# Performance work log

Measured on AMD Instinct MI355X. Metric: run time of the kernel, lower is better.

The kernel has to match this reference:

```python
import jax, jax.numpy as jnp
import numpy as np

B, N, E = 64, 128, 262144
HID, NRBF, NBLK = 128, 64, 4
RCUT = 6.0
GAMMA = 10.0 / (RCUT * RCUT)


def setup_inputs() -> dict:
    key = jax.random.key(0)
    ks = jax.random.split(key, 20)
    s_rbf = 1.0 / np.sqrt(NRBF)
    s_hid = 1.0 / np.sqrt(HID)
    return {
        "Z": jax.random.randint(ks[0], (B, N), 0, 100),
        "pos": jax.random.normal(ks[1], (B, N, 3), dtype=jnp.float32) * 3.0,
        "edge_index": jax.random.randint(ks[2], (2, E), 0, B * N),
        "embed_w": jax.random.normal(ks[3], (100, HID), dtype=jnp.float32) * 0.02,
        "edge_w1": jax.random.normal(ks[4], (NBLK, NRBF, HID), dtype=jnp.float32) * s_rbf,
        "edge_b1": jnp.zeros((NBLK, HID), dtype=jnp.float32),
        "edge_w2": jax.random.normal(ks[5], (NBLK, HID, HID), dtype=jnp.float32) * s_hid,
        "edge_b2": jnp.zeros((NBLK, HID), dtype=jnp.float32),
        "lin_in_w": jax.random.normal(ks[6], (NBLK, HID, HID), dtype=jnp.float32) * s_hid,
        "node_w1": jax.random.normal(ks[7], (NBLK, HID, HID), dtype=jnp.float32) * s_hid,
        "node_b1": jnp.zeros((NBLK, HID), dtype=jnp.float32),
        "node_w2": jax.random.normal(ks[8], (NBLK, HID, HID), dtype=jnp.float32) * s_hid,
        "node_b2": jnp.zeros((NBLK, HID), dtype=jnp.float32),
        "ln_g": jnp.ones((NBLK, HID), dtype=jnp.float32),
        "ln_b": jnp.zeros((NBLK, HID), dtype=jnp.float32),
        "ro_w1": jax.random.normal(ks[9], (HID, HID // 2), dtype=jnp.float32) * s_hid,
        "ro_b1": jnp.zeros((HID // 2,), dtype=jnp.float32),
        "ro_w2": jax.random.normal(ks[10], (HID // 2, 1), dtype=jnp.float32) * (1.0 / np.sqrt(HID // 2)),
        "ro_b2": jnp.zeros((1,), dtype=jnp.float32),
    }


def _layernorm(x, g, b, eps=1e-5):
    mu = x.mean(-1, keepdims=True)
    var = ((x - mu) ** 2).mean(-1, keepdims=True)
    return (x - mu) / jnp.sqrt(var + eps) * g + b


def reference(Z, pos, edge_index, embed_w, edge_w1, edge_b1, edge_w2, edge_b2,
              lin_in_w, node_w1, node_b1, node_w2, node_b2, ln_g, ln_b,
              ro_w1, ro_b1, ro_w2, ro_b2):
    Zf = Z.reshape(-1)               # [B*N]
    pf = pos.reshape(-1, 3)          # [B*N, 3]
    src, dst = edge_index[0], edge_index[1]

    h = embed_w[Zf]                  # [B*N, H]

    # edge RBF features
    d = jnp.linalg.norm(pf[src] - pf[dst], axis=-1)      # [E]
    d = jnp.minimum(d, RCUT)
    centers = jnp.linspace(0.0, RCUT, NRBF)
    rbf = jnp.exp(-GAMMA * (d[:, None] - centers) ** 2)  # [E, NRBF]

    for i in range(NBLK):
        # CFConv: edge filter MLP on rbf
        w = jax.nn.silu(rbf @ edge_w1[i] + edge_b1[i]) @ edge_w2[i] + edge_b2[i]  # [E,H]
        m = w * (h[src] @ lin_in_w[i])                                            # [E,H]
        agg = jnp.zeros_like(h).at[dst].add(m)                                    # scatter-add [B*N,H]
        out = jax.nn.silu(agg @ node_w1[i] + node_b1[i]) @ node_w2[i] + node_b2[i]
        h = _layernorm(h + out, ln_g[i], ln_b[i])

    # readout: SiLU -> Linear -> SiLU -> Linear
    x = jax.nn.silu(h) @ ro_w1 + ro_b1
    e_atom = (jax.nn.silu(x) @ ro_w2 + ro_b2)[:, 0]      # [B*N]
    return e_atom.reshape(B, N).sum(axis=-1)             # per-graph energies [B]
```

## Files before the change

kernel.cpp:

```cpp
#include <hip/hip_runtime.h>

#define BN 8192
#define EE 262144
#define HIDD 128
#define NRBF 64
#define NBLK 4
#define TLUT 2048
#define CAP 128
#define MR 16
#define FR 8
#define RCUTF 6.0f
#define GAMMAF (10.0f / 36.0f)

typedef unsigned short u16;
typedef __attribute__((ext_vector_type(8))) short short8x;
typedef __attribute__((ext_vector_type(4))) float f32x4;

__device__ __forceinline__ float silu_f(float v) {
    return v / (1.0f + __expf(-v));
}
__device__ __forceinline__ float bf2f(u16 u) {
    return __uint_as_float(((unsigned)u) << 16);
}
__device__ __forceinline__ u16 f2bf(float f) {
    unsigned u = __float_as_uint(f);
    unsigned r = u + 0x7FFFu + ((u >> 16) & 1u);
    return (u16)(r >> 16);
}

__global__ void k_prep(const float* __restrict__ liw, const float* __restrict__ nw1,
                       const float* __restrict__ nw2, const float* __restrict__ ro1,
                       u16* __restrict__ liwT, u16* __restrict__ nw1T,
                       u16* __restrict__ nw2T, u16* __restrict__ ro1T,
                       int* __restrict__ cnt, float* __restrict__ out, int out_n) {
    int id0 = blockIdx.x * 256 + threadIdx.x;
    for (int id = id0; id < 12 * 16384; id += 65536) {
        int which = id >> 14;
        int r = id & 16383;
        int n = r >> 7, k = r & 127;
        const float* src = which < 4 ? liw : (which < 8 ? nw1 : nw2);
        u16* dst = which < 4 ? liwT : (which < 8 ? nw1T : nw2T);
        int b = which & 3;
        dst[b * 16384 + n * 128 + k] = f2bf(src[(size_t)b * 16384 + k * 128 + n]);
    }
    if (id0 < 8192) {
        cnt[id0] = 0;
        int n = id0 >> 7, k = id0 & 127;
        ro1T[n * 128 + k] = f2bf(ro1[k * 64 + n]);
        if (id0 < out_n) out[id0] = 0.0f;
    }
}

__global__ void k_edges(const int* __restrict__ ei, const float* __restrict__ pos,
                        int* __restrict__ cnt, int* __restrict__ meta) {
    int e = blockIdx.x * 256 + threadIdx.x;
    int s = ei[e];
    int d = ei[EE + e];
    float dx = pos[s * 3 + 0] - pos[d * 3 + 0];
    float dy = pos[s * 3 + 1] - pos[d * 3 + 1];
    float dz = pos[s * 3 + 2] - pos[d * 3 + 2];
    float dist = fminf(sqrtf(dx * dx + dy * dy + dz * dz), RCUTF);
    int i0 = (int)(dist * ((TLUT - 1) / RCUTF) + 0.5f);
    i0 = i0 > TLUT - 1 ? TLUT - 1 : i0;
    int p = atomicAdd(&cnt[d], 1);
    if (p < CAP) meta[(size_t)d * CAP + p] = (i0 << 13) | s;
}

__global__ __launch_bounds__(256) void k_lutall(const float* __restrict__ W1a,
                                                const float* __restrict__ b1a,
                                                const float* __restrict__ W2a,
                                                const float* __restrict__ b2a,
                                                u16* __restrict__ lutall) {
    __shared__ float As[32 * 33];
    __shared__ float Ws[32 * 128];
    __shared__ float T2[32 * 128];
    int net = blockIdx.x >> 6;
    int r0l = (blockIdx.x & 63) * 32;
    const float* W1 = W1a + (size_t)net * NRBF * HIDD;
    const float* b1 = b1a + net * HIDD;
    const float* W2 = W2a + (size_t)net * HIDD * HIDD;
    const float* b2 = b2a + net * HIDD;
    u16* lutp = lutall + (size_t)net * TLUT * HIDD;
    int tid = threadIdx.x;
    int tx = tid & 31, ty = tid >> 5;
    int c0 = tx * 4, rr = ty * 4;
    float acc[4][4] = {};
    for (int kc = 0; kc < NRBF; kc += 32) {
        int lr = tid >> 3, lc = (tid & 7) * 4;
        float dt = (r0l + lr) * (RCUTF / (TLUT - 1));
#pragma unroll
        for (int j = 0; j < 4; ++j) {
            float c = (kc + lc + j) * (RCUTF / 63.0f);
            float u = dt - c;
            As[lr * 33 + lc + j] = __expf(-GAMMAF * u * u);
        }
#pragma unroll
        for (int j = 0; j < 4; ++j) {
            int idx = tid + j * 256;
            int wr = idx >> 5, wc = (idx & 31) * 4;
            *(float4*)&Ws[wr * 128 + wc] =
                *(const float4*)&W1[(size_t)(kc + wr) * HIDD + wc];
        }
        __syncthreads();
#pragma unroll 8
        for (int k = 0; k < 32; ++k) {
            float4 wv = *(float4*)&Ws[k * 128 + c0];
            float a0 = As[(rr + 0) * 33 + k];
            float a1 = As[(rr + 1) * 33 + k];
            float a2 = As[(rr + 2) * 33 + k];
            float a3 = As[(rr + 3) * 33 + k];
            acc[0][0] += a0 * wv.x; acc[0][1] += a0 * wv.y; acc[0][2] += a0 * wv.z; acc[0][3] += a0 * wv.w;
            acc[1][0] += a1 * wv.x; acc[1][1] += a1 * wv.y; acc[1][2] += a1 * wv.z; acc[1][3] += a1 * wv.w;
            acc[2][0] += a2 * wv.x; acc[2][1] += a2 * wv.y; acc[2][2] += a2 * wv.z; acc[2][3] += a2 * wv.w;
            acc[3][0] += a3 * wv.x; acc[3][1] += a3 * wv.y; acc[3][2] += a3 * wv.z; acc[3][3] += a3 * wv.w;
        }
        __syncthreads();
    }
#pragma unroll
    for (int i = 0; i < 4; ++i)
#pragma unroll
        for (int j = 0; j < 4; ++j)
            T2[(rr + i) * 128 + c0 + j] = silu_f(acc[i][j] + b1[c0 + j]);
    float acc2[4][4] = {};
    __syncthreads();
    for (int kc = 0; kc < HIDD; kc += 32) {
#pragma unroll
        for (int j = 0; j < 4; ++j) {
            int idx = tid + j * 256;
            int wr = idx >> 5, wc = (idx & 31) * 4;
            *(float4*)&Ws[wr * 128 + wc] =
                *(const float4*)&W2[(size_t)(kc + wr) * HIDD + wc];
        }
        __syncthreads();
#pragma unroll 8
        for (int k = 0; k < 32; ++k) {
            float4 wv = *(float4*)&Ws[k * 128 + c0];
            float a0 = T2[(rr + 0) * 128 + kc + k];
            float a1 = T2[(rr + 1) * 128 + kc + k];
            float a2 = T2[(rr + 2) * 128 + kc + k];
            float a3 = T2[(rr + 3) * 128 + kc + k];
            acc2[0][0] += a0 * wv.x; acc2[0][1] += a0 * wv.y; acc2[0][2] += a0 * wv.z; acc2[0][3] += a0 * wv.w;
            acc2[1][0] += a1 * wv.x; acc2[1][1] += a1 * wv.y; acc2[1][2] += a1 * wv.z; acc2[1][3] += a1 * wv.w;
            acc2[2][0] += a2 * wv.x; acc2[2][1] += a2 * wv.y; acc2[2][2] += a2 * wv.z; acc2[2][3] += a2 * wv.w;
            acc2[3][0] += a3 * wv.x; acc2[3][1] += a3 * wv.y; acc2[3][2] += a3 * wv.z; acc2[3][3] += a3 * wv.w;
        }
        __syncthreads();
    }
#pragma unroll
    for (int i = 0; i < 4; ++i) {
        int t = r0l + rr + i;
        ushort4 o;
        o.x = f2bf(acc2[i][0] + b2[c0 + 0]);
        o.y = f2bf(acc2[i][1] + b2[c0 + 1]);
        o.z = f2bf(acc2[i][2] + b2[c0 + 2]);
        o.w = f2bf(acc2[i][3] + b2[c0 + 3]);
        *(ushort4*)&lutp[(size_t)t * HIDD + c0] = o;
    }
}

__global__ __launch_bounds__(256, 2) void k_embedx(const int* __restrict__ Z,
                                                   const float* __restrict__ ew,
                                                   const u16* __restrict__ liwT0,
                                                   float* __restrict__ h,
                                                   u16* __restrict__ xb) {
    __shared__ u16 Wt[128][136];
    __shared__ u16 Ab[MR][136];
    int tid = threadIdx.x;
    int r0 = blockIdx.x * MR;
    {
        int row = tid >> 4, c8 = (tid & 15) * 8;
        int z = Z[r0 + row];
        const float* er = ew + (size_t)z * HIDD + c8;
        float* hr = h + (size_t)(r0 + row) * HIDD + c8;
        float4 v0 = *(const float4*)er;
        float4 v1 = *(const float4*)(er + 4);
        *(float4*)hr = v0;
        *(float4*)(hr + 4) = v1;
        ushort4 a0, a1;
        a0.x = f2bf(v0.x); a0.y = f2bf(v0.y); a0.z = f2bf(v0.z); a0.w = f2bf(v0.w);
        a1.x = f2bf(v1.x); a1.y = f2bf(v1.y); a1.z = f2bf(v1.z); a1.w = f2bf(v1.w);
        *(ushort4*)&Ab[row][c8] = a0;
        *(ushort4*)&Ab[row][c8 + 4] = a1;
    }
    for (int idx = tid; idx < 2048; idx += 256) {
        int r = idx >> 4, c = (idx & 15) * 8;
        *(float4*)&Wt[r][c] = *(const float4*)&liwT0[r * HIDD + c];
    }
    __syncthreads();
    int w = tid >> 6, l = tid & 63;
    int m = l & 15, q4 = l >> 4, q8 = q4 * 8;
    f32x4 a0 = {0, 0, 0, 0}, a1 = {0, 0, 0, 0};
#pragma unroll
    for (int kc = 0; kc < 128; kc += 32) {
        short8x av = *(const short8x*)&Ab[m][kc + q8];
        short8x b0 = *(const short8x*)&Wt[w * 32 + m][kc + q8];
        short8x b1 = *(const short8x*)&Wt[w * 32 + 16 + m][kc + q8];
        a0 = __builtin_amdgcn_mfma_f32_16x16x32_bf16(av, b0, a0, 0, 0, 0);
        a1 = __builtin_amdgcn_mfma_f32_16x16x32_bf16(av, b1, a1, 0, 0, 0);
    }
    int c = w * 32 + m;
#pragma unroll
    for (int r = 0; r < 4; ++r) {
        int row = q4 * 4 + r;
        u16* xr = xb + (size_t)(r0 + row) * HIDD;
        xr[c] = f2bf(a0[r]);
        xr[c + 16] = f2bf(a1[r]);
    }
}

__global__ __launch_bounds__(512, 6) void k_fiter(
    const int* __restrict__ cnt, const int* __restrict__ meta,
    const u16* __restrict__ lut, const u16* __restrict__ xin,
    float* __restrict__ h,
    const u16* __restrict__ w1t, const float* __restrict__ b1,
    const u16* __restrict__ w2t, const float* __restrict__ b2,
    const float* __restrict__ g, const float* __restrict__ bb,
    const u16* __restrict__ w3t, u16* __restrict__ xout, int last,
    const float* __restrict__ rb1, const float* __restrict__ rw2,
    const float* __restrict__ rb2, float* __restrict__ out) {
    __shared__ u16 SH[2176 + 128 * 136];
    __shared__ float RED[152];
    int tid = threadIdx.x;
    int w = tid >> 6, l = tid & 63;
    int m = l & 15, q4 = l >> 4, q8 = q4 * 8;
    int r0 = blockIdx.x * FR;
    u16* Ab = SH;
    u16* Tb = SH + 1088;
    u16* Wt = SH + 2176;

    {
        int dst = r0 + w;
        int n = cnt[dst];
        n = n > CAP ? CAP : n;
        const int* mp = meta + (size_t)dst * CAP;
        int nm1 = n > 0 ? n - 1 : 0;
        int mA = mp[l < nm1 ? l : nm1];
        int mB = mp[64 + l < nm1 ? 64 + l : nm1];
        float ax = 0.0f, ay = 0.0f;
#pragma unroll 4
        for (int t = 0; t < n; ++t) {
            int md = __shfl(t < 64 ? mA : mB, t & 63);
            int s = md & 8191;
            int i0 = md >> 13;
            ushort2 lv = *(const ushort2*)&lut[((size_t)i0 << 7) + 2 * l];
            ushort2 xv = *(const ushort2*)&xin[((size_t)s << 7) + 2 * l];
            ax = fmaf(bf2f(lv.x), bf2f(xv.x), ax);
            ay = fmaf(bf2f(lv.y), bf2f(xv.y), ay);
        }
        ushort2 o;
        o.x = f2bf(ax);
        o.y = f2bf(ay);
        *(ushort2*)&Ab[w * 136 + 2 * l] = o;
    }
    for (int idx = tid; idx < 2048; idx += 512) {
        int r = idx >> 4, c = (idx & 15) * 8;
        *(float4*)&Wt[r * 136 + c] = *(const float4*)&w1t[r * HIDD + c];
    }
    __syncthreads();

    int col = w * 16 + m;
    f32x4 ac1 = {0, 0, 0, 0};
#pragma unroll
    for (int kc = 0; kc < 128; kc += 32) {
        short8x av = *(const short8x*)&Ab[m * 136 + kc + q8];
        short8x bv = *(const short8x*)&Wt[(w * 16 + m) * 136 + kc + q8];
        ac1 = __builtin_amdgcn_mfma_f32_16x16x32_bf16(av, bv, ac1, 0, 0, 0);
    }
    __syncthreads();
    {
        float bv = b1[col];
        if (q4 < 2) {
#pragma unroll
            for (int r = 0; r < 4; ++r)
                Tb[(q4 * 4 + r) * 136 + col] = f2bf(silu_f(ac1[r] + bv));
        }
    }
    for (int idx = tid; idx < 2048; idx += 512) {
        int r = idx >> 4, c = (idx & 15) * 8;
        *(float4*)&Wt[r * 136 + c] = *(const float4*)&w2t[r * HIDD + c];
    }
    __syncthreads();

    f32x4 ac2 = {0, 0, 0, 0};
#pragma unroll
    for (int kc = 0; kc < 128; kc += 32) {
        short8x av = *(const short8x*)&Tb[m * 136 + kc + q8];
        short8x bv = *(const short8x*)&Wt[(w * 16 + m) * 136 + kc + q8];
        ac2 = __builtin_amdgcn_mfma_f32_16x16x32_bf16(av, bv, ac2, 0, 0, 0);
    }
    float v[4], sS = 0.0f, sQ = 0.0f;
    if (q4 < 2) {
        float bv = b2[col];
#pragma unroll
        for (int r = 0; r < 4; ++r) {
            int row = q4 * 4 + r;
            v[r] = ac2[r] + bv + h[(size_t)(r0 + row) * HIDD + col];
        }
    }
    __syncthreads();

    if (q4 < 2) {
#pragma unroll
        for (int r = 0; r < 4; ++r) {
            float s = v[r], q = v[r] * v[r];
#pragma unroll
            for (int mm = 1; mm < 16; mm <<= 1) {
                s += __shfl_xor(s, mm);
                q += __shfl_xor(q, mm);
            }
            if (m == 0) {
                RED[w * 8 + q4 * 4 + r] = s;
                RED[64 + w * 8 + q4 * 4 + r] = q;
            }
        }
    }
    {
        int rows3 = last ? 64 : 128;
        for (int idx = tid; idx < rows3 * 16; idx += 512) {
            int r = idx >> 4, c = (idx & 15) * 8;
            *(float4*)&Wt[r * 136 + c] = *(const float4*)&w3t[r * HIDD + c];
        }
    }
    __syncthreads();
    if (tid < 8) {
        float s = 0.0f, q = 0.0f;
#pragma unroll
        for (int ww = 0; ww < 8; ++ww) {
            s += RED[ww * 8 + tid];
            q += RED[64 + ww * 8 + tid];
        }
        float mu = s * (1.0f / 128.0f);
        float var = q * (1.0f / 128.0f) - mu * mu;
        RED[128 + tid] = mu;
        RED[136 + tid] = rsqrtf(var + 1e-5f);
    }
    __syncthreads();
    if (q4 < 2) {
        float gv = g[col], bbv = bb[col];
#pragma unroll
        for (int r = 0; r < 4; ++r) {
            int row = q4 * 4 + r;
            float mu = RED[128 + row], rs = RED[136 + row];
            float o = (v[r] - mu) * rs * gv + bbv;
            if (!last) h[(size_t)(r0 + row) * HIDD + col] = o;
            Ab[row * 136 + col] = f2bf(last ? silu_f(o) : o);
        }
    }
    __syncthreads();

    if (!last) {
        f32x4 ac3 = {0, 0, 0, 0};
#pragma unroll
        for (int kc = 0; kc < 128; kc += 32) {
            short8x av = *(const short8x*)&Ab[m * 136 + kc + q8];
            short8x bv = *(const short8x*)&Wt[(w * 16 + m) * 136 + kc + q8];
            ac3 = __builtin_amdgcn_mfma_f32_16x16x32_bf16(av, bv, ac3, 0, 0, 0);
        }
        if (q4 < 2) {
#pragma unroll
            for (int r = 0; r < 4; ++r) {
                int row = q4 * 4 + r;
                xout[(size_t)(r0 + row) * HIDD + col] = f2bf(ac3[r]);
            }
        }
    } else {
        float tsum = 0.0f;
        if (w < 4) {
            f32x4 ac3 = {0, 0, 0, 0};
#pragma unroll
            for (int kc = 0; kc < 128; kc += 32) {
                short8x av = *(const short8x*)&Ab[m * 136 + kc + q8];
                short8x bv = *(const short8x*)&Wt[(w * 16 + m) * 136 + kc + q8];
                ac3 = __builtin_amdgcn_mfma_f32_16x16x32_bf16(av, bv, ac3, 0, 0, 0);
            }
            if (q4 < 2) {
                float bv = rb1[col], wv = rw2[col];
#pragma unroll
                for (int r = 0; r < 4; ++r) tsum += silu_f(ac3[r] + bv) * wv;
            }
#pragma unroll
            for (int mm = 1; mm < 64; mm <<= 1) tsum += __shfl_xor(tsum, mm);
            if (l == 0) RED[144 + w] = tsum;
        }
        __syncthreads();
        if (tid == 0) {
            float tot = RED[144] + RED[145] + RED[146] + RED[147] +
                        (float)FR * rb2[0];
            atomicAdd(&out[blockIdx.x >> 4], tot);
        }
    }
}

extern "C" void kernel_launch(void* const* d_in, const int* in_sizes, int n_in,
                              void* d_out, int out_size, void* d_ws, size_t ws_size,
                              hipStream_t stream) {
    const int*   Z   = (const int*)d_in[0];
    const float* pos = (const float*)d_in[1];
    const int*   ei  = (const int*)d_in[2];
    const float* ew  = (const float*)d_in[3];
    const float* ew1 = (const float*)d_in[4];
    const float* eb1 = (const float*)d_in[5];
    const float* ew2 = (const float*)d_in[6];
    const float* eb2 = (const float*)d_in[7];
    const float* liw = (const float*)d_in[8];
    const float* nw1 = (const float*)d_in[9];
    const float* nb1 = (const float*)d_in[10];
    const float* nw2 = (const float*)d_in[11];
    const float* nb2 = (const float*)d_in[12];
    const float* lng = (const float*)d_in[13];
    const float* lnb = (const float*)d_in[14];
    const float* rw1 = (const float*)d_in[15];
    const float* rb1 = (const float*)d_in[16];
    const float* rw2 = (const float*)d_in[17];
    const float* rb2 = (const float*)d_in[18];
    float* out = (float*)d_out;

    float* h      = (float*)d_ws;
    u16*   xb0    = (u16*)(h + (size_t)BN * HIDD);
    u16*   xb1    = xb0 + (size_t)BN * HIDD;
    u16*   lutall = xb1 + (size_t)BN * HIDD;
    u16*   liwT   = lutall + (size_t)NBLK * TLUT * HIDD;
    u16*   nw1T   = liwT + (size_t)NBLK * HIDD * HIDD;
    u16*   nw2T   = nw1T + (size_t)NBLK * HIDD * HIDD;
    u16*   ro1T   = nw2T + (size_t)NBLK * HIDD * HIDD;
    int*   cnt    = (int*)(ro1T + 64 * HIDD);
    int*   meta   = (int*)(cnt + BN);

    k_prep<<<256, 256, 0, stream>>>(liw, nw1, nw2, rw1, liwT, nw1T, nw2T, ro1T,
                                    cnt, out, out_size);
    k_edges<<<EE / 256, 256, 0, stream>>>(ei, pos, cnt, meta);
    k_lutall<<<NBLK * (TLUT / 32), 256, 0, stream>>>(ew1, eb1, ew2, eb2, lutall);
    k_embedx<<<BN / MR, 256, 0, stream>>>(Z, ew, liwT, h, xb0);

    u16* xbuf[2] = {xb0, xb1};
    for (int i = 0; i < NBLK; ++i) {
        int last = (i == NBLK - 1);
        k_fiter<<<BN / FR, 512, 0, stream>>>(
            cnt, meta, lutall + (size_t)i * TLUT * HIDD, xbuf[i & 1], h,
            nw1T + (size_t)i * HIDD * HIDD, nb1 + i * HIDD,
            nw2T + (size_t)i * HIDD * HIDD, nb2 + i * HIDD,
            lng + i * HIDD, lnb + i * HIDD,
            last ? ro1T : liwT + (size_t)(i + 1) * HIDD * HIDD,
            last ? (u16*)nullptr : xbuf[(i + 1) & 1],
            last, rb1, rw2, rb2, out);
    }
}
```

Measured before the change: 231.1 us.

## Merge setup kernels and vectorize edge gather with 4-way edge parallelism

Merges the prep and edge-binning kernels into one launch, and the LUT build and embedding projection into another union-shared-memory launch. The count buffer is now cleared with a memset. This cuts launch count and lets independent setup work run concurrently. The per-node edge aggregation in k_fiter now has each lane load 8 bf16 values with 16-byte vector loads, processes four edges in parallel across lane quarters, and reduces them with shuffles. Occupancy hint drops from 6 to 4 blocks per SM to make room for the larger register footprint.

```diff
diff --git a/kernel.cpp b/kernel.cpp
--- a/kernel.cpp
+++ b/kernel.cpp
@@ -14,6 +14,7 @@
 
 typedef unsigned short u16;
 typedef __attribute__((ext_vector_type(8))) short short8x;
+typedef __attribute__((ext_vector_type(8))) unsigned short u16x8;
 typedef __attribute__((ext_vector_type(4))) float f32x4;
 
 __device__ __forceinline__ float silu_f(float v) {
@@ -28,13 +29,28 @@
     return (u16)(r >> 16);
 }
 
-__global__ void k_prep(const float* __restrict__ liw, const float* __restrict__ nw1,
-                       const float* __restrict__ nw2, const float* __restrict__ ro1,
-                       u16* __restrict__ liwT, u16* __restrict__ nw1T,
-                       u16* __restrict__ nw2T, u16* __restrict__ ro1T,
-                       int* __restrict__ cnt, float* __restrict__ out, int out_n) {
-    int id0 = blockIdx.x * 256 + threadIdx.x;
-    for (int id = id0; id < 12 * 16384; id += 65536) {
+__global__ void k_pe(const int* __restrict__ ei, const float* __restrict__ pos,
+                     const float* __restrict__ liw, const float* __restrict__ nw1,
+                     const float* __restrict__ nw2, const float* __restrict__ ro1,
+                     int* __restrict__ cnt, int* __restrict__ meta,
+                     u16* __restrict__ liwT, u16* __restrict__ nw1T,
+                     u16* __restrict__ nw2T, u16* __restrict__ ro1T,
+                     float* __restrict__ out, int out_n) {
+    int tid = threadIdx.x, blk = blockIdx.x;
+    if (blk < 1024) {
+        int e = blk * 256 + tid;
+        int s = ei[e];
+        int d = ei[EE + e];
+        float dx = pos[s * 3 + 0] - pos[d * 3 + 0];
+        float dy = pos[s * 3 + 1] - pos[d * 3 + 1];
+        float dz = pos[s * 3 + 2] - pos[d * 3 + 2];
+        float dist = fminf(sqrtf(dx * dx + dy * dy + dz * dz), RCUTF);
+        int i0 = (int)(dist * ((TLUT - 1) / RCUTF) + 0.5f);
+        i0 = i0 > TLUT - 1 ? TLUT - 1 : i0;
+        int p = atomicAdd(&cnt[d], 1);
+        if (p < CAP) meta[(size_t)d * CAP + p] = (i0 << 13) | s;
+    } else if (blk < 1792) {
+        int id = (blk - 1024) * 256 + tid;
         int which = id >> 14;
         int r = id & 16383;
         int n = r >> 7, k = r & 127;
@@ -42,173 +58,153 @@
         u16* dst = which < 4 ? liwT : (which < 8 ? nw1T : nw2T);
         int b = which & 3;
         dst[b * 16384 + n * 128 + k] = f2bf(src[(size_t)b * 16384 + k * 128 + n]);
-    }
-    if (id0 < 8192) {
-        cnt[id0] = 0;
-        int n = id0 >> 7, k = id0 & 127;
-        ro1T[n * 128 + k] = f2bf(ro1[k * 64 + n]);
-        if (id0 < out_n) out[id0] = 0.0f;
-    }
-}
-
-__global__ void k_edges(const int* __restrict__ ei, const float* __restrict__ pos,
-                        int* __restrict__ cnt, int* __restrict__ meta) {
-    int e = blockIdx.x * 256 + threadIdx.x;
-    int s = ei[e];
-    int d = ei[EE + e];
-    float dx = pos[s * 3 + 0] - pos[d * 3 + 0];
-    float dy = pos[s * 3 + 1] - pos[d * 3 + 1];
-    float dz = pos[s * 3 + 2] - pos[d * 3 + 2];
-    float dist = fminf(sqrtf(dx * dx + dy * dy + dz * dz), RCUTF);
-    int i0 = (int)(dist * ((TLUT - 1) / RCUTF) + 0.5f);
-    i0 = i0 > TLUT - 1 ? TLUT - 1 : i0;
-    int p = atomicAdd(&cnt[d], 1);
-    if (p < CAP) meta[(size_t)d * CAP + p] = (i0 << 13) | s;
-}
-
-__global__ __launch_bounds__(256) void k_lutall(const float* __restrict__ W1a,
-                                                const float* __restrict__ b1a,
-                                                const float* __restrict__ W2a,
-                                                const float* __restrict__ b2a,
-                                                u16* __restrict__ lutall) {
-    __shared__ float As[32 * 33];
-    __shared__ float Ws[32 * 128];
-    __shared__ float T2[32 * 128];
-    int net = blockIdx.x >> 6;
-    int r0l = (blockIdx.x & 63) * 32;
-    const float* W1 = W1a + (size_t)net * NRBF * HIDD;
-    const float* b1 = b1a + net * HIDD;
-    const float* W2 = W2a + (size_t)net * HIDD * HIDD;
-    const float* b2 = b2a + net * HIDD;
-    u16* lutp = lutall + (size_t)net * TLUT * HIDD;
-    int tid = threadIdx.x;
-    int tx = tid & 31, ty = tid >> 5;
-    int c0 = tx * 4, rr = ty * 4;
-    float acc[4][4] = {};
-    for (int kc = 0; kc < NRBF; kc += 32) {
-        int lr = tid >> 3, lc = (tid & 7) * 4;
-        float dt = (r0l + lr) * (RCUTF / (TLUT - 1));
-#pragma unroll
-        for (int j = 0; j < 4; ++j) {
-            float c = (kc + lc + j) * (RCUTF / 63.0f);
-            float u = dt - c;
-            As[lr * 33 + lc + j] = __expf(-GAMMAF * u * u);
-        }
-#pragma unroll
-        for (int j = 0; j < 4; ++j) {
-            int idx = tid + j * 256;
-            int wr = idx >> 5, wc = (idx & 31) * 4;
-            *(float4*)&Ws[wr * 128 + wc] =
-                *(const float4*)&W1[(size_t)(kc + wr) * HIDD + wc];
-        }
+    } else {
+        int id = (blk - 1792) * 256 + tid;
+        int n = id >> 7, k = id & 127;
+        ro1T[n * 128 + k] = f2bf(ro1[(size_t)k * 64 + n]);
+        if (blk == 1792 && tid < out_n) out[tid] = 0.0f;
+    }
+}
+
+__global__ __launch_bounds__(256, 2) void k_le(
+    const float* __restrict__ W1a, const float* __restrict__ b1a,
+    const float* __restrict__ W2a, const float* __restrict__ b2a,
+    u16* __restrict__ lutall,
+    const int* __restrict__ Z, const float* __restrict__ ew,
+    const u16* __restrict__ liwT0, float* __restrict__ h,
+    u16* __restrict__ xb) {
+    __shared__ union {
+        struct { float As[32 * 33]; float Ws[32 * 128]; float T2[32 * 128]; } lu;
+        struct { u16 Wt[128][136]; u16 Ab[MR][136]; } ex;
+    } S;
+    int tid = threadIdx.x, blk = blockIdx.x;
+    if (blk < 256) {
+        int net = blk >> 6;
+        int r0l = (blk & 63) * 32;
+        const float* W1 = W1a + (size_t)net * NRBF * HIDD;
+        const float* b1 = b1a + net * HIDD;
+        const float* W2 = W2a + (size_t)net * HIDD * HIDD;
+        const float* b2 = b2a + net * HIDD;
+        u16* lutp = lutall + (size_t)net * TLUT * HIDD;
+        int tx = tid & 31, ty = tid >> 5;
+        int c0 = tx * 4, rr = ty * 4;
+        float acc[4][4] = {};
+        for (int kc = 0; kc < NRBF; kc += 32) {
+            int lr = tid >> 3, lc = (tid & 7) * 4;
+            float dt = (r0l + lr) * (RCUTF / (TLUT - 1));
+#pragma unroll
+            for (int j = 0; j < 4; ++j) {
+                float c = (kc + lc + j) * (RCUTF / 63.0f);
+                float u = dt - c;
+                S.lu.As[lr * 33 + lc + j] = __expf(-GAMMAF * u * u);
+            }
+#pragma unroll
+            for (int j = 0; j < 4; ++j) {
+                int idx = tid + j * 256;
+                int wr = idx >> 5, wc = (idx & 31) * 4;
+                *(float4*)&S.lu.Ws[wr * 128 + wc] =
+                    *(const float4*)&W1[(size_t)(kc + wr) * HIDD + wc];
+            }
+            __syncthreads();
+#pragma unroll 8
+            for (int k = 0; k < 32; ++k) {
+                float4 wv = *(float4*)&S.lu.Ws[k * 128 + c0];
+                float a0 = S.lu.As[(rr + 0) * 33 + k];
+                float a1 = S.lu.As[(rr + 1) * 33 + k];
+                float a2 = S.lu.As[(rr + 2) * 33 + k];
+                float a3 = S.lu.As[(rr + 3) * 33 + k];
+                acc[0][0] += a0 * wv.x; acc[0][1] += a0 * wv.y; acc[0][2] += a0 * wv.z; acc[0][3] += a0 * wv.w;
+                acc[1][0] += a1 * wv.x; acc[1][1] += a1 * wv.y; acc[1][2] += a1 * wv.z; acc[1][3] += a1 * wv.w;
+                acc[2][0] += a2 * wv.x; acc[2][1] += a2 * wv.y; acc[2][2] += a2 * wv.z; acc[2][3] += a2 * wv.w;
+                acc[3][0] += a3 * wv.x; acc[3][1] += a3 * wv.y; acc[3][2] += a3 * wv.z; acc[3][3] += a3 * wv.w;
+            }
+            __syncthreads();
+        }
+#pragma unroll
+        for (int i = 0; i < 4; ++i)
+#pragma unroll
+            for (int j = 0; j < 4; ++j)
+                S.lu.T2[(rr + i) * 128 + c0 + j] = silu_f(acc[i][j] + b1[c0 + j]);
+        float acc2[4][4] = {};
         __syncthreads();
+        for (int kc = 0; kc < HIDD; kc += 32) {
+#pragma unroll
+            for (int j = 0; j < 4; ++j) {
+                int idx = tid + j * 256;
+                int wr = idx >> 5, wc = (idx & 31) * 4;
+                *(float4*)&S.lu.Ws[wr * 128 + wc] =
+                    *(const float4*)&W2[(size_t)(kc + wr) * HIDD + wc];
+            }
+            __syncthreads();
 #pragma unroll 8
-        for (int k = 0; k < 32; ++k) {
-            float4 wv = *(float4*)&Ws[k * 128 + c0];
-            float a0 = As[(rr + 0) * 33 + k];
-            float a1 = As[(rr + 1) * 33 + k];
-            float a2 = As[(rr + 2) * 33 + k];
-            float a3 = As[(rr + 3) * 33 + k];
-            acc[0][0] += a0 * wv.x; acc[0][1] += a0 * wv.y; acc[0][2] += a0 * wv.z; acc[0][3] += a0 * wv.w;
-            acc[1][0] += a1 * wv.x; acc[1][1] += a1 * wv.y; acc[1][2] += a1 * wv.z; acc[1][3] += a1 * wv.w;
-            acc[2][0] += a2 * wv.x; acc[2][1] += a2 * wv.y; acc[2][2] += a2 * wv.z; acc[2][3] += a2 * wv.w;
-            acc[3][0] += a3 * wv.x; acc[3][1] += a3 * wv.y; acc[3][2] += a3 * wv.z; acc[3][3] += a3 * wv.w;
+            for (int k = 0; k < 32; ++k) {
+                float4 wv = *(float4*)&S.lu.Ws[k * 128 + c0];
+                float a0 = S.lu.T2[(rr + 0) * 128 + kc + k];
+                float a1 = S.lu.T2[(rr + 1) * 128 + kc + k];
+                float a2 = S.lu.T2[(rr + 2) * 128 + kc + k];
+                float a3 = S.lu.T2[(rr + 3) * 128 + kc + k];
+                acc2[0][0] += a0 * wv.x; acc2[0][1] += a0 * wv.y; acc2[0][2] += a0 * wv.z; acc2[0][3] += a0 * wv.w;
+                acc2[1][0] += a1 * wv.x; acc2[1][1] += a1 * wv.y; acc2[1][2] += a1 * wv.z; acc2[1][3] += a1 * wv.w;
+                acc2[2][0] += a2 * wv.x; acc2[2][1] += a2 * wv.y; acc2[2][2] += a2 * wv.z; acc2[2][3] += a2 * wv.w;
+                acc2[3][0] += a3 * wv.x; acc2[3][1] += a3 * wv.y; acc2[3][2] += a3 * wv.z; acc2[3][3] += a3 * wv.w;
+            }
+            __syncthreads();
+        }
+#pragma unroll
+        for (int i = 0; i < 4; ++i) {
+            int t = r0l + rr + i;
+            ushort4 o;
+            o.x = f2bf(acc2[i][0] + b2[c0 + 0]);
+            o.y = f2bf(acc2[i][1] + b2[c0 + 1]);
+            o.z = f2bf(acc2[i][2] + b2[c0 + 2]);
+            o.w = f2bf(acc2[i][3] + b2[c0 + 3]);
+            *(ushort4*)&lutp[(size_t)t * HIDD + c0] = o;
+        }
+    } else {
+        int r0 = (blk - 256) * MR;
+        {
+            int row = tid >> 4, c8 = (tid & 15) * 8;
+            int z = Z[r0 + row];
+            const float* er = ew + (size_t)z * HIDD + c8;
+            float* hr = h + (size_t)(r0 + row) * HIDD + c8;
+            float4 v0 = *(const float4*)er;
+            float4 v1 = *(const float4*)(er + 4);
+            *(float4*)hr = v0;
+            *(float4*)(hr + 4) = v1;
+            ushort4 a0, a1;
+            a0.x = f2bf(v0.x); a0.y = f2bf(v0.y); a0.z = f2bf(v0.z); a0.w = f2bf(v0.w);
+            a1.x = f2bf(v1.x); a1.y = f2bf(v1.y); a1.z = f2bf(v1.z); a1.w = f2bf(v1.w);
+            *(ushort4*)&S.ex.Ab[row][c8] = a0;
+            *(ushort4*)&S.ex.Ab[row][c8 + 4] = a1;
+        }
+        for (int idx = tid; idx < 2048; idx += 256) {
+            int r = idx >> 4, c = (idx & 15) * 8;
+            *(float4*)&S.ex.Wt[r][c] = *(const float4*)&liwT0[r * HIDD + c];
         }
         __syncthreads();
-    }
-#pragma unroll
-    for (int i = 0; i < 4; ++i)
-#pragma unroll
-        for (int j = 0; j < 4; ++j)
-            T2[(rr + i) * 128 + c0 + j] = silu_f(acc[i][j] + b1[c0 + j]);
-    float acc2[4][4] = {};
-    __syncthreads();
-    for (int kc = 0; kc < HIDD; kc += 32) {
-#pragma unroll
-        for (int j = 0; j < 4; ++j) {
-            int idx = tid + j * 256;
-            int wr = idx >> 5, wc = (idx & 31) * 4;
-            *(float4*)&Ws[wr * 128 + wc] =
-                *(const float4*)&W2[(size_t)(kc + wr) * HIDD + wc];
-        }
-        __syncthreads();
-#pragma unroll 8
-        for (int k = 0; k < 32; ++k) {
-            float4 wv = *(float4*)&Ws[k * 128 + c0];
-            float a0 = T2[(rr + 0) * 128 + kc + k];
-            float a1 = T2[(rr + 1) * 128 + kc + k];
-            float a2 = T2[(rr + 2) * 128 + kc + k];
-            float a3 = T2[(rr + 3) * 128 + kc + k];
-            acc2[0][0] += a0 * wv.x; acc2[0][1] += a0 * wv.y; acc2[0][2] += a0 * wv.z; acc2[0][3] += a0 * wv.w;
-            acc2[1][0] += a1 * wv.x; acc2[1][1] += a1 * wv.y; acc2[1][2] += a1 * wv.z; acc2[1][3] += a1 * wv.w;
-            acc2[2][0] += a2 * wv.x; acc2[2][1] += a2 * wv.y; acc2[2][2] += a2 * wv.z; acc2[2][3] += a2 * wv.w;
-            acc2[3][0] += a3 * wv.x; acc2[3][1] += a3 * wv.y; acc2[3][2] += a3 * wv.z; acc2[3][3] += a3 * wv.w;
-        }
-        __syncthreads();
-    }
-#pragma unroll
-    for (int i = 0; i < 4; ++i) {
-        int t = r0l + rr + i;
-        ushort4 o;
-        o.x = f2bf(acc2[i][0] + b2[c0 + 0]);
-        o.y = f2bf(acc2[i][1] + b2[c0 + 1]);
-        o.z = f2bf(acc2[i][2] + b2[c0 + 2]);
-        o.w = f2bf(acc2[i][3] + b2[c0 + 3]);
-        *(ushort4*)&lutp[(size_t)t * HIDD + c0] = o;
-    }
-}
-
-__global__ __launch_bounds__(256, 2) void k_embedx(const int* __restrict__ Z,
-                                                   const float* __restrict__ ew,
-                                                   const u16* __restrict__ liwT0,
-                                                   float* __restrict__ h,
-                                                   u16* __restrict__ xb) {
-    __shared__ u16 Wt[128][136];
-    __shared__ u16 Ab[MR][136];
-    int tid = threadIdx.x;
-    int r0 = blockIdx.x * MR;
-    {
-        int row = tid >> 4, c8 = (tid & 15) * 8;
-        int z = Z[r0 + row];
-        const float* er = ew + (size_t)z * HIDD + c8;
-        float* hr = h + (size_t)(r0 + row) * HIDD + c8;
-        float4 v0 = *(const float4*)er;
-        float4 v1 = *(const float4*)(er + 4);
-        *(float4*)hr = v0;
-        *(float4*)(hr + 4) = v1;
-        ushort4 a0, a1;
-        a0.x = f2bf(v0.x); a0.y = f2bf(v0.y); a0.z = f2bf(v0.z); a0.w = f2bf(v0.w);
-        a1.x = f2bf(v1.x); a1.y = f2bf(v1.y); a1.z = f2bf(v1.z); a1.w = f2bf(v1.w);
-        *(ushort4*)&Ab[row][c8] = a0;
-        *(ushort4*)&Ab[row][c8 + 4] = a1;
-    }
-    for (int idx = tid; idx < 2048; idx += 256) {
-        int r = idx >> 4, c = (idx & 15) * 8;
-        *(float4*)&Wt[r][c] = *(const float4*)&liwT0[r * HIDD + c];
-    }
-    __syncthreads();
-    int w = tid >> 6, l = tid & 63;
-    int m = l & 15, q4 = l >> 4, q8 = q4 * 8;
-    f32x4 a0 = {0, 0, 0, 0}, a1 = {0, 0, 0, 0};
-#pragma unroll
-    for (int kc = 0; kc < 128; kc += 32) {
-        short8x av = *(const short8x*)&Ab[m][kc + q8];
-        short8x b0 = *(const short8x*)&Wt[w * 32 + m][kc + q8];
-        short8x b1 = *(const short8x*)&Wt[w * 32 + 16 + m][kc + q8];
-        a0 = __builtin_amdgcn_mfma_f32_16x16x32_bf16(av, b0, a0, 0, 0, 0);
-        a1 = __builtin_amdgcn_mfma_f32_16x16x32_bf16(av, b1, a1, 0, 0, 0);
-    }
-    int c = w * 32 + m;
-#pragma unroll
-    for (int r = 0; r < 4; ++r) {
-        int row = q4 * 4 + r;
-        u16* xr = xb + (size_t)(r0 + row) * HIDD;
-        xr[c] = f2bf(a0[r]);
-        xr[c + 16] = f2bf(a1[r]);
-    }
-}
-
-__global__ __launch_bounds__(512, 6) void k_fiter(
+        int w = tid >> 6, l = tid & 63;
+        int m = l & 15, q4 = l >> 4, q8 = q4 * 8;
+        f32x4 a0 = {0, 0, 0, 0}, a1 = {0, 0, 0, 0};
+#pragma unroll
+        for (int kc = 0; kc < 128; kc += 32) {
+            short8x av = *(const short8x*)&S.ex.Ab[m][kc + q8];
+            short8x b0 = *(const short8x*)&S.ex.Wt[w * 32 + m][kc + q8];
+            short8x b1 = *(const short8x*)&S.ex.Wt[w * 32 + 16 + m][kc + q8];
+            a0 = __builtin_amdgcn_mfma_f32_16x16x32_bf16(av, b0, a0, 0, 0, 0);
+            a1 = __builtin_amdgcn_mfma_f32_16x16x32_bf16(av, b1, a1, 0, 0, 0);
+        }
+        int c = w * 32 + m;
+#pragma unroll
+        for (int r = 0; r < 4; ++r) {
+            int row = q4 * 4 + r;
+            u16* xr = xb + (size_t)(r0 + row) * HIDD;
+            xr[c] = f2bf(a0[r]);
+            xr[c + 16] = f2bf(a1[r]);
+        }
+    }
+}
+
+__global__ __launch_bounds__(512, 4) void k_fiter(
     const int* __restrict__ cnt, const int* __restrict__ meta,
     const u16* __restrict__ lut, const u16* __restrict__ xin,
     float* __restrict__ h,
@@ -236,21 +232,33 @@
         int nm1 = n > 0 ? n - 1 : 0;
         int mA = mp[l < nm1 ? l : nm1];
         int mB = mp[64 + l < nm1 ? 64 + l : nm1];
-        float ax = 0.0f, ay = 0.0f;
-#pragma unroll 4
-        for (int t = 0; t < n; ++t) {
-            int md = __shfl(t < 64 ? mA : mB, t & 63);
-            int s = md & 8191;
-            int i0 = md >> 13;
-            ushort2 lv = *(const ushort2*)&lut[((size_t)i0 << 7) + 2 * l];
-            ushort2 xv = *(const ushort2*)&xin[((size_t)s << 7) + 2 * l];
-            ax = fmaf(bf2f(lv.x), bf2f(xv.x), ax);
-            ay = fmaf(bf2f(lv.y), bf2f(xv.y), ay);
-        }
-        ushort2 o;
-        o.x = f2bf(ax);
-        o.y = f2bf(ay);
-        *(ushort2*)&Ab[w * 136 + 2 * l] = o;
+        float ax[8] = {};
+        int tmax = (n + 3) >> 2;
+#pragma unroll 2
+        for (int t = 0; t < tmax; ++t) {
+            int e4 = t * 4 + q4;
+            int md = __shfl(e4 < 64 ? mA : mB, e4 & 63);
+            if (e4 < n) {
+                int s = md & 8191;
+                int i0 = md >> 13;
+                u16x8 lv = *(const u16x8*)&lut[((size_t)i0 << 7) + 8 * m];
+                u16x8 xv = *(const u16x8*)&xin[((size_t)s << 7) + 8 * m];
+#pragma unroll
+                for (int j = 0; j < 8; ++j)
+                    ax[j] = fmaf(bf2f(lv[j]), bf2f(xv[j]), ax[j]);
+            }
+        }
+#pragma unroll
+        for (int j = 0; j < 8; ++j) {
+            ax[j] += __shfl_xor(ax[j], 16);
+            ax[j] += __shfl_xor(ax[j], 32);
+        }
+        if (q4 == 0) {
+            u16x8 o;
+#pragma unroll
+            for (int j = 0; j < 8; ++j) o[j] = f2bf(ax[j]);
+            *(u16x8*)&Ab[w * 136 + 8 * m] = o;
+        }
     }
     for (int idx = tid; idx < 2048; idx += 512) {
         int r = idx >> 4, c = (idx & 15) * 8;
@@ -288,7 +296,7 @@
         short8x bv = *(const short8x*)&Wt[(w * 16 + m) * 136 + kc + q8];
         ac2 = __builtin_amdgcn_mfma_f32_16x16x32_bf16(av, bv, ac2, 0, 0, 0);
     }
-    float v[4], sS = 0.0f, sQ = 0.0f;
+    float v[4];
     if (q4 < 2) {
         float bv = b2[col];
 #pragma unroll
@@ -426,11 +434,12 @@
     int*   cnt    = (int*)(ro1T + 64 * HIDD);
     int*   meta   = (int*)(cnt + BN);
 
-    k_prep<<<256, 256, 0, stream>>>(liw, nw1, nw2, rw1, liwT, nw1T, nw2T, ro1T,
-                                    cnt, out, out_size);
-    k_edges<<<EE / 256, 256, 0, stream>>>(ei, pos, cnt, meta);
-    k_lutall<<<NBLK * (TLUT / 32), 256, 0, stream>>>(ew1, eb1, ew2, eb2, lutall);
-    k_embedx<<<BN / MR, 256, 0, stream>>>(Z, ew, liwT, h, xb0);
+    (void)hipMemsetAsync(cnt, 0, BN * sizeof(int), stream);
+    k_pe<<<1824, 256, 0, stream>>>(ei, pos, liw, nw1, nw2, rw1,
+                                   cnt, meta, liwT, nw1T, nw2T, ro1T,
+                                   out, out_size);
+    k_le<<<768, 256, 0, stream>>>(ew1, eb1, ew2, eb2, lutall,
+                                  Z, ew, liwT, h, xb0);
 
     u16* xbuf[2] = {xb0, xb1};
     for (int i = 0; i < NBLK; ++i) {
```

Result: faster. 210.2 us (-9.0%).
